# Optimization experiments

Hardware: AMD Instinct MI355X
Metric: run time of the kernel (lower is better)

## Reference

```python
import jax, jax.numpy as jnp
import numpy as np

CLUSTERS = 128
ITERATIONS = 10
TOPK = 32
NEG = -1e7


def setup_inputs() -> dict:
    key = jax.random.key(0)
    k1, k2, k3, k4 = jax.random.split(key, 4)
    N, L, H, E = 2, 2048, 8, 64
    BITS = 32
    return {
        "queries": jax.random.normal(k1, (N, L, H, E), dtype=jnp.float32),
        "keys": jax.random.normal(k2, (N, L, H, E), dtype=jnp.float32),
        "values": jax.random.normal(k3, (N, L, H, E), dtype=jnp.float32),
        "planes": jax.random.normal(k4, (BITS, E + 1), dtype=jnp.float32),
    }


def _cluster(bits, C, iterations):
    # bits: [N,H,L,B] in {0,1}. Lloyd k-means under Hamming distance.
    N, H, L, B = bits.shape
    init_idx = (np.arange(C) * L) // C
    cent = bits[:, :, init_idx, :]  # [N,H,C,B]
    for _ in range(iterations):
        # hamming(b,c) = b.(1-c) + (1-b).c
        d = (jnp.einsum('nhlb,nhcb->nhlc', bits, 1.0 - cent)
             + jnp.einsum('nhlb,nhcb->nhlc', 1.0 - bits, cent))
        assign = jnp.argmin(d, axis=-1)                      # [N,H,L]
        oh = jax.nn.one_hot(assign, C, dtype=jnp.float32)    # [N,H,L,C]
        cnt = oh.sum(axis=2)                                 # [N,H,C]
        sums = jnp.einsum('nhlc,nhlb->nhcb', oh, bits)
        new = (sums / jnp.maximum(cnt, 1.0)[..., None] >= 0.5).astype(jnp.float32)
        cent = jnp.where((cnt > 0.0)[..., None], new, cent)
    d = (jnp.einsum('nhlb,nhcb->nhlc', bits, 1.0 - cent)
         + jnp.einsum('nhlb,nhcb->nhlc', 1.0 - bits, cent))
    assign = jnp.argmin(d, axis=-1)
    oh = jax.nn.one_hot(assign, C, dtype=jnp.float32)
    cnt = oh.sum(axis=2)
    return assign, oh, cnt


def _forward(queries, keys, values, planes):
    # to [N,H,L,E]
    Q = jnp.transpose(queries, (0, 2, 1, 3))
    K = jnp.transpose(keys, (0, 2, 1, 3))
    V = jnp.transpose(values, (0, 2, 1, 3))
    N, H, L, E = Q.shape
    S = K.shape[2]
    temp = 1.0 / np.sqrt(E)

    # --- hash queries with random hyperplanes (bias column: hash_bias=True) ---
    x = jnp.concatenate([Q, jnp.ones(Q.shape[:-1] + (1,), Q.dtype)], axis=-1)
    bits = (jnp.einsum('nhle,be->nhlb', x, planes) > 0).astype(jnp.float32)

    # --- cluster queries (Lloyd on hamming distance over hash bits) ---
    assign, oh, cnt = _cluster(bits, CLUSTERS, ITERATIONS)

    # --- per-cluster centroid queries (mean over members) ---
    Qg = jnp.einsum('nhlc,nhle->nhce', oh, Q) / jnp.maximum(cnt, 1.0)[..., None]

    # --- top-k keys per cluster ---
    QKc = jnp.einsum('nhce,nhse->nhcs', Qg, K)   # [N,H,C,S]
    k = min(TOPK, S)
    _, tki = jax.lax.top_k(QKc, k)               # [N,H,C,k]

    # broadcast each cluster's top-k indices to its member queries
    idx_q = jnp.take_along_axis(
        tki, jnp.broadcast_to(assign[:, :, :, None], (N, H, L, k)), axis=2)  # [N,H,L,k]

    gather = jax.vmap(jax.vmap(lambda a, i: a[i]))
    K_sel = gather(K, idx_q)                     # [N,H,L,k,E]
    V_sel = gather(V, idx_q)                     # [N,H,L,k,E]

    qk = jnp.einsum('nhle,nhlke->nhlk', Q, K_sel)
    future = idx_q > jnp.arange(L)[None, None, :, None]   # causal: key pos > query pos
    qk = jnp.where(future, NEG, qk)
    A = jax.nn.softmax(temp * qk, axis=-1)
    A = A * (1.0 - future.astype(A.dtype))
    out = jnp.einsum('nhlk,nhlkd->nhld', A, V_sel)
    return jnp.transpose(out, (0, 2, 1, 3))      # [N,L,H,D]


def reference(queries, keys, values, planes):
    return _forward(queries, keys, values, planes)
```

## Files before the change

kernel.cpp:

```cpp
#include <hip/hip_runtime.h>
#include <math.h>

#define NB 2
#define HB 8
#define LB 2048
#define EB 64
#define BITSN 32
#define CLN 128
#define ITERS 10
#define TOPKN 32
#define NEGV -10000000.0f

typedef unsigned long long u64;
typedef unsigned int u32;

#define PART_NH16 (33 * 64)
#define PART_ITER16 (NB * HB * PART_NH16)
#define PART_TOTAL16 (ITERS * PART_ITER16)
#define BITS_BLOCKS 4096
#define ZBLOCKS ((PART_TOTAL16 + 255) / 256)

__global__ __launch_bounds__(256) void bits_zero_kernel(const float* __restrict__ q,
                                                        const float* __restrict__ planes,
                                                        u32* __restrict__ bits,
                                                        u32* __restrict__ zbuf) {
    int tid = threadIdx.x;
    int bid = blockIdx.x;
    if (bid >= BITS_BLOCKS) {
        int i = (bid - BITS_BLOCKS) * 256 + tid;
        if (i < PART_TOTAL16) zbuf[i] = 0u;
        return;
    }
    int wave = tid >> 6;
    int lane = tid & 63;
    int b = lane & 31;
    int which = lane >> 5;
    int qi = bid * 8 + wave * 2 + which;
    int l = qi & (LB - 1);
    int nh = qi / LB;
    int h = nh & (HB - 1);
    int n = nh / HB;
    const float* qrow = q + (((long long)n * LB + l) * HB + h) * EB;
    const float* prow = planes + b * (EB + 1);
    double acc = (double)prow[EB];
    #pragma unroll 8
    for (int e = 0; e < EB; ++e) acc += (double)qrow[e] * (double)prow[e];
    unsigned long long m = __ballot(acc > 0.0);
    if (b == 0) {
        bits[qi] = (u32)(which ? (m >> 32) : (m & 0xffffffffULL));
    }
}

__global__ __launch_bounds__(256) void kmeans_iter_kernel(const u32* __restrict__ bits,
                                                          const u32* __restrict__ part_prev,
                                                          u32* __restrict__ part_cur,
                                                          const u32* __restrict__ cent_prev_g,
                                                          u32* __restrict__ cent_cur_g,
                                                          int it) {
    __shared__ u32 cent[CLN];
    __shared__ int hist[33 * 128];
    int tid = threadIdx.x;
    int bid = blockIdx.x;
    int nh = bid >> 3;
    int tile = bid & 7;
    int lane = tid & 63;

    for (int i = tid; i < 33 * 128; i += 256) hist[i] = 0;
    if (tid < CLN) {
        u32 cv;
        if (it == 0) {
            cv = bits[nh * LB + tid * (LB / CLN)];
        } else {
            const u32* pp = part_prev + nh * PART_NH16;
            int sh = (tid & 1) * 16;
            int cnt = (int)((pp[32 * 64 + (tid >> 1)] >> sh) & 0xffffu);
            u32 nb = 0u;
            #pragma unroll
            for (int j = 0; j < BITSN; ++j) {
                int s = (int)((pp[j * 64 + (tid >> 1)] >> sh) & 0xffffu);
                if (2 * s >= cnt) nb |= (1u << j);
            }
            cv = (cnt > 0) ? nb : cent_prev_g[nh * CLN + tid];
        }
        cent[tid] = cv;
        if (tile == 0) cent_cur_g[nh * CLN + tid] = cv;
    }
    __syncthreads();

    int l = tile * 256 + tid;
    u32 bv = bits[nh * LB + l];

    u32 clo = cent[lane], chi = cent[lane + 64];
    u32 best = 0x7fffffffu;
    #pragma unroll 16
    for (int c = 0; c < 64; ++c) {
        u32 cc = (u32)__builtin_amdgcn_readlane((int)clo, c);
        u32 key = ((u32)__popc(bv ^ cc) << 7) | (u32)c;
        best = (key < best) ? key : best;
    }
    #pragma unroll 16
    for (int c = 0; c < 64; ++c) {
        u32 cc = (u32)__builtin_amdgcn_readlane((int)chi, c);
        u32 key = ((u32)__popc(bv ^ cc) << 7) | (u32)(64 + c);
        best = (key < best) ? key : best;
    }
    int bc = (int)(best & 127u);

    atomicAdd(&hist[32 * 128 + bc], 1);
    u32 bb = bv;
    while (bb) { int j = __ffs(bb) - 1; atomicAdd(&hist[j * 128 + bc], 1); bb &= bb - 1; }
    __syncthreads();

    u32* pc = part_cur + nh * PART_NH16;
    for (int i = tid; i < PART_NH16; i += 256) {
        int j = i >> 6, p = i & 63;
        u32 v = (u32)hist[j * 128 + 2 * p] | ((u32)hist[j * 128 + 2 * p + 1] << 16);
        if (v) atomicAdd(&pc[i], v);
    }
}

__global__ __launch_bounds__(1024) void list_final_kernel(const u32* __restrict__ bits,
                                                          const u32* __restrict__ part_prev,
                                                          const u32* __restrict__ cent_prev_g,
                                                          int* __restrict__ csort_g,
                                                          int* __restrict__ cnt_g,
                                                          int* __restrict__ ofs_g,
                                                          int* __restrict__ list_g) {
    __shared__ u32 cent[CLN];
    __shared__ int cnt[CLN];
    __shared__ int cntw[2][16][CLN];
    __shared__ int ofs[CLN];
    int nh = blockIdx.x;
    int tid = threadIdx.x;
    int w = tid >> 6, lane = tid & 63;

    if (tid < CLN) {
        const u32* pp = part_prev + nh * PART_NH16;
        int sh = (tid & 1) * 16;
        int cn = (int)((pp[32 * 64 + (tid >> 1)] >> sh) & 0xffffu);
        u32 nb = 0u;
        #pragma unroll
        for (int j = 0; j < BITSN; ++j) {
            int s = (int)((pp[j * 64 + (tid >> 1)] >> sh) & 0xffffu);
            if (2 * s >= cn) nb |= (1u << j);
        }
        cent[tid] = (cn > 0) ? nb : cent_prev_g[nh * CLN + tid];
        cnt[tid] = 0;
    }
    for (int i = tid; i < 2 * 16 * CLN; i += 1024) (&cntw[0][0][0])[i] = 0;
    __syncthreads();

    int l0 = tid, l1 = tid + 1024;
    u32 bv0 = bits[nh * LB + l0];
    u32 bv1 = bits[nh * LB + l1];
    u32 clo = cent[lane], chi = cent[lane + 64];
    u32 best0 = 0x7fffffffu, best1 = 0x7fffffffu;
    #pragma unroll 16
    for (int c = 0; c < 64; ++c) {
        u32 cc = (u32)__builtin_amdgcn_readlane((int)clo, c);
        u32 k0 = ((u32)__popc(bv0 ^ cc) << 7) | (u32)c;
        u32 k1 = ((u32)__popc(bv1 ^ cc) << 7) | (u32)c;
        best0 = (k0 < best0) ? k0 : best0;
        best1 = (k1 < best1) ? k1 : best1;
    }
    #pragma unroll 16
    for (int c = 0; c < 64; ++c) {
        u32 cc = (u32)__builtin_amdgcn_readlane((int)chi, c);
        u32 k0 = ((u32)__popc(bv0 ^ cc) << 7) | (u32)(64 + c);
        u32 k1 = ((u32)__popc(bv1 ^ cc) << 7) | (u32)(64 + c);
        best0 = (k0 < best0) ? k0 : best0;
        best1 = (k1 < best1) ? k1 : best1;
    }
    int bc0 = (int)(best0 & 127u);
    int bc1 = (int)(best1 & 127u);
    u64 ltmask = (lane == 0) ? 0ULL : (~0ULL >> (64 - lane));

    int rank0 = 0, rank1 = 0;
    for (int c = 0; c < CLN; ++c) {
        u64 m0 = __ballot(bc0 == c);
        u64 m1 = __ballot(bc1 == c);
        if ((m0 | m1) == 0ULL) continue;
        if (bc0 == c) rank0 = (int)__popcll(m0 & ltmask);
        if (bc1 == c) rank1 = (int)__popcll(m1 & ltmask);
        if (lane == 0) {
            int p0 = (int)__popcll(m0), p1 = (int)__popcll(m1);
            if (p0) cntw[0][w][c] = p0;
            if (p1) cntw[1][w][c] = p1;
            atomicAdd(&cnt[c], p0 + p1);
        }
    }
    __syncthreads();
    if (tid == 0) {
        int run = 0;
        for (int c = 0; c < CLN; ++c) { ofs[c] = run; run += cnt[c]; }
    }
    __syncthreads();
    if (tid < CLN) {
        int c = tid;
        int run = ofs[c];
        #pragma unroll
        for (int g = 0; g < 2; ++g)
            for (int ww = 0; ww < 16; ++ww) {
                int t = cntw[g][ww][c];
                cntw[g][ww][c] = run;
                run += t;
            }
        cnt_g[nh * CLN + c] = cnt[c];
        ofs_g[nh * CLN + c] = ofs[c];
    }
    __syncthreads();
    {
        int p0 = cntw[0][w][bc0] + rank0;
        int p1 = cntw[1][w][bc1] + rank1;
        list_g[nh * LB + p0] = l0;
        list_g[nh * LB + p1] = l1;
        csort_g[nh * LB + p0] = bc0;
        csort_g[nh * LB + p1] = bc1;
    }
}

__global__ __launch_bounds__(256) void qg_kernel(const float* __restrict__ q,
                                                 const int* __restrict__ cnt_g,
                                                 const int* __restrict__ ofs_g,
                                                 const int* __restrict__ list_g,
                                                 float* __restrict__ qgf) {
    __shared__ double ps[4][EB];
    int bid = blockIdx.x;
    int nh = bid >> 7;
    int h = nh & (HB - 1);
    int n = nh / HB;
    int tid = threadIdx.x;
    int w = tid >> 6, lane = tid & 63;
    int cn = cnt_g[bid];
    int o = ofs_g[bid];
    const int* lp = list_g + nh * LB + o;
    double acc = 0.0;
    for (int i = w; i < cn; i += 4) {
        int l = lp[i];
        acc += (double)q[(((long long)n * LB + l) * HB + h) * EB + lane];
    }
    ps[w][lane] = acc;
    __syncthreads();
    if (tid < EB) {
        double s = ((ps[0][tid] + ps[1][tid]) + ps[2][tid]) + ps[3][tid];
        double dcn = (double)(cn > 0 ? cn : 1);
        qgf[(long long)bid * EB + tid] = (float)(s / dcn);
    }
}

__global__ __launch_bounds__(256) void scores_kernel(const float* __restrict__ kk,
                                                     const float* __restrict__ qgf,
                                                     u32* __restrict__ keys) {
    __shared__ float qs[CLN * EB];
    int bid = blockIdx.x;
    int nh = bid >> 5;
    int tile = bid & 31;
    int h = nh & (HB - 1);
    int n = nh / HB;
    int tid = threadIdx.x;
    int w = tid >> 6;
    int lane = tid & 63;
    int l = tile * 64 + lane;
    int cbase = w * 32;

    {
        const float4* src = (const float4*)(qgf + (long long)nh * CLN * EB);
        float4* dst = (float4*)qs;
        #pragma unroll
        for (int i = 0; i < 8; ++i) dst[tid + 256 * i] = src[tid + 256 * i];
    }

    const float4* kr4 = (const float4*)(kk + (((long long)n * LB + l) * HB + h) * EB);
    float rr[EB];
    #pragma unroll
    for (int i = 0; i < 16; ++i) {
        float4 t4 = kr4[i];
        rr[4 * i] = t4.x; rr[4 * i + 1] = t4.y; rr[4 * i + 2] = t4.z; rr[4 * i + 3] = t4.w;
    }
    __syncthreads();

    for (int c = 0; c < 32; ++c) {
        const float4* qp = (const float4*)(qs + (cbase + c) * EB);
        float a0 = 0.f, a1 = 0.f, a2 = 0.f, a3 = 0.f;
        #pragma unroll
        for (int i = 0; i < 4; ++i) {
            float4 q0 = qp[i], q1 = qp[4 + i], q2 = qp[8 + i], q3 = qp[12 + i];
            int e0 = 4 * i, e1 = 16 + 4 * i, e2 = 32 + 4 * i, e3 = 48 + 4 * i;
            a0 = fmaf(q0.x, rr[e0], a0); a0 = fmaf(q0.y, rr[e0 + 1], a0);
            a0 = fmaf(q0.z, rr[e0 + 2], a0); a0 = fmaf(q0.w, rr[e0 + 3], a0);
            a1 = fmaf(q1.x, rr[e1], a1); a1 = fmaf(q1.y, rr[e1 + 1], a1);
            a1 = fmaf(q1.z, rr[e1 + 2], a1); a1 = fmaf(q1.w, rr[e1 + 3], a1);
            a2 = fmaf(q2.x, rr[e2], a2); a2 = fmaf(q2.y, rr[e2 + 1], a2);
            a2 = fmaf(q2.z, rr[e2 + 2], a2); a2 = fmaf(q2.w, rr[e2 + 3], a2);
            a3 = fmaf(q3.x, rr[e3], a3); a3 = fmaf(q3.y, rr[e3 + 1], a3);
            a3 = fmaf(q3.z, rr[e3 + 2], a3); a3 = fmaf(q3.w, rr[e3 + 3], a3);
        }
        float acc = (a0 + a1) + (a2 + a3);
        u32 u = __float_as_uint(acc);
        u = ((int)u < 0) ? ~u : (u | 0x80000000u);
        keys[((long long)(nh * CLN + cbase + c)) * LB + l] = u;
    }
}

__global__ __launch_bounds__(64) void topsel_kernel(const u32* __restrict__ keys,
                                                    int* __restrict__ tki_g) {
    int bid = blockIdx.x;
    int lane = threadIdx.x;
    const uint4* kp4 = (const uint4*)(keys + (long long)bid * LB);
    u64 k[32];
    #pragma unroll
    for (int t = 0; t < 8; ++t) {
        uint4 kv = kp4[lane + 64 * t];
        int l0 = (lane + 64 * t) * 4;
        k[4 * t]     = ((u64)kv.x << 32) | (u32)(2047 - l0);
        k[4 * t + 1] = ((u64)kv.y << 32) | (u32)(2047 - (l0 + 1));
        k[4 * t + 2] = ((u64)kv.z << 32) | (u32)(2047 - (l0 + 2));
        k[4 * t + 3] = ((u64)kv.w << 32) | (u32)(2047 - (l0 + 3));
    }
    u64 m0 = k[0], m1 = k[8], m2 = k[16], m3 = k[24];
    #pragma unroll
    for (int t = 1; t < 8; ++t) {
        if (k[t] > m0) m0 = k[t];
        if (k[8 + t] > m1) m1 = k[8 + t];
        if (k[16 + t] > m2) m2 = k[16 + t];
        if (k[24 + t] > m3) m3 = k[24 + t];
    }
    if (m1 > m0) m0 = m1;
    if (m3 > m2) m2 = m3;
    u64 cur = (m2 > m0) ? m2 : m0;

    for (int r = 0; r < TOPKN; ++r) {
        u64 wk = cur;
        #pragma unroll
        for (int off = 1; off < 64; off <<= 1) {
            u64 o = __shfl_xor(wk, off);
            if (o > wk) wk = o;
        }
        if (lane == 0) tki_g[bid * TOPKN + r] = 2047 - (int)(wk & 2047u);
        if (wk == cur) {
            u64 nm = 0ULL;
            #pragma unroll
            for (int t = 0; t < 32; ++t) {
                u64 kt = k[t];
                u64 cand = (kt < wk) ? kt : 0ULL;
                if (cand > nm) nm = cand;
            }
            cur = nm;
        }
    }
}

__device__ __forceinline__ void attn_one(const float* __restrict__ q,
                                         const float* __restrict__ kk,
                                         const float* __restrict__ vv,
                                         int n, int h, int l,
                                         const int* __restrict__ krow,
                                         int lane, float* __restrict__ out) {
    int j = lane & 31, p = lane >> 5;
    int kidx = krow[j];
    const float* vbase = vv + ((long long)n * LB * HB + h) * EB;
    float vreg[TOPKN];
    #pragma unroll
    for (int jj = 0; jj < TOPKN; ++jj) {
        int kj = __shfl(kidx, jj);
        vreg[jj] = vbase[(long long)kj * (HB * EB) + lane];
    }
    const float4* q4 = (const float4*)(q + (((long long)n * LB + l) * HB + h) * EB) + p * 8;
    const float4* k4 = (const float4*)(kk + (((long long)n * LB + kidx) * HB + h) * EB) + p * 8;
    float part = 0.f;
    #pragma unroll
    for (int i = 0; i < 8; ++i) {
        float4 a = q4[i], b = k4[i];
        part += a.x * b.x + a.y * b.y + a.z * b.z + a.w * b.w;
    }
    float qlo = __shfl(part, j);
    float qhi = __shfl(part, j + 32);
    float qk = qlo + qhi;
    bool future = kidx > l;
    float logit = 0.125f * (future ? NEGV : qk);
    float m = logit;
    #pragma unroll
    for (int off = 16; off; off >>= 1) m = fmaxf(m, __shfl_xor(m, off));
    float ex = expf(logit - m);
    float ssum = ex;
    #pragma unroll
    for (int off = 16; off; off >>= 1) ssum += __shfl_xor(ssum, off);
    float a = future ? 0.f : ex / ssum;
    float oacc = 0.f;
    #pragma unroll
    for (int jj = 0; jj < TOPKN; ++jj) {
        float aj = __shfl(a, jj);
        oacc = fmaf(aj, vreg[jj], oacc);
    }
    out[(((long long)n * LB + l) * HB + h) * EB + lane] = oacc;
}

__global__ __launch_bounds__(256) void attn_quad_kernel(const float* __restrict__ q,
                                                        const float* __restrict__ kk,
                                                        const float* __restrict__ vv,
                                                        const int* __restrict__ list_g,
                                                        const int* __restrict__ csort_g,
                                                        const int* __restrict__ tki_g,
                                                        float* __restrict__ out) {
    int tid = threadIdx.x;
    int wave = tid >> 6, lane = tid & 63;
    int idx = blockIdx.x * 4 + wave;
    int nh = idx >> 9;
    int qd = idx & 511;
    int pos = 4 * qd;
    int l0 = list_g[nh * LB + pos];
    int l1 = list_g[nh * LB + pos + 1];
    int l2 = list_g[nh * LB + pos + 2];
    int l3 = list_g[nh * LB + pos + 3];
    int c0 = csort_g[nh * LB + pos];
    int c1 = csort_g[nh * LB + pos + 1];
    int c2 = csort_g[nh * LB + pos + 2];
    int c3 = csort_g[nh * LB + pos + 3];
    int h = nh & (HB - 1);
    int n = nh / HB;

    if ((c0 != c1) | (c1 != c2) | (c2 != c3)) {
        attn_one(q, kk, vv, n, h, l0, tki_g + (nh * CLN + c0) * TOPKN, lane, out);
        attn_one(q, kk, vv, n, h, l1, tki_g + (nh * CLN + c1) * TOPKN, lane, out);
        attn_one(q, kk, vv, n, h, l2, tki_g + (nh * CLN + c2) * TOPKN, lane, out);
        attn_one(q, kk, vv, n, h, l3, tki_g + (nh * CLN + c3) * TOPKN, lane, out);
        return;
    }

    const int* krow = tki_g + (nh * CLN + c0) * TOPKN;
    int j = lane & 31, p = lane >> 5;
    int kidx = krow[j];
    const float* vbase = vv + ((long long)n * LB * HB + h) * EB;
    float vreg[TOPKN];
    #pragma unroll
    for (int jj = 0; jj < TOPKN; ++jj) {
        int kj = __shfl(kidx, jj);
        vreg[jj] = vbase[(long long)kj * (HB * EB) + lane];
    }

    const float4* q40 = (const float4*)(q + (((long long)n * LB + l0) * HB + h) * EB) + p * 8;
    const float4* q41 = (const float4*)(q + (((long long)n * LB + l1) * HB + h) * EB) + p * 8;
    const float4* q42 = (const float4*)(q + (((long long)n * LB + l2) * HB + h) * EB) + p * 8;
    const float4* q43 = (const float4*)(q + (((long long)n * LB + l3) * HB + h) * EB) + p * 8;
    const float4* k4  = (const float4*)(kk + (((long long)n * LB + kidx) * HB + h) * EB) + p * 8;
    float p0 = 0.f, p1 = 0.f, p2 = 0.f, p3 = 0.f;
    #pragma unroll
    for (int i = 0; i < 8; ++i) {
        float4 b = k4[i];
        float4 a0 = q40[i], a1 = q41[i], a2 = q42[i], a3 = q43[i];
        p0 += a0.x * b.x + a0.y * b.y + a0.z * b.z + a0.w * b.w;
        p1 += a1.x * b.x + a1.y * b.y + a1.z * b.z + a1.w * b.w;
        p2 += a2.x * b.x + a2.y * b.y + a2.z * b.z + a2.w * b.w;
        p3 += a3.x * b.x + a3.y * b.y + a3.z * b.z + a3.w * b.w;
    }
    float qk0 = __shfl(p0, j) + __shfl(p0, j + 32);
    float qk1 = __shfl(p1, j) + __shfl(p1, j + 32);
    float qk2 = __shfl(p2, j) + __shfl(p2, j + 32);
    float qk3 = __shfl(p3, j) + __shfl(p3, j + 32);

    bool f0 = kidx > l0, f1 = kidx > l1, f2 = kidx > l2, f3 = kidx > l3;
    float g0 = 0.125f * (f0 ? NEGV : qk0);
    float g1 = 0.125f * (f1 ? NEGV : qk1);
    float g2 = 0.125f * (f2 ? NEGV : qk2);
    float g3 = 0.125f * (f3 ? NEGV : qk3);
    float m0 = g0, m1 = g1, m2 = g2, m3 = g3;
    #pragma unroll
    for (int off = 16; off; off >>= 1) {
        m0 = fmaxf(m0, __shfl_xor(m0, off));
        m1 = fmaxf(m1, __shfl_xor(m1, off));
        m2 = fmaxf(m2, __shfl_xor(m2, off));
        m3 = fmaxf(m3, __shfl_xor(m3, off));
    }
    float e0 = expf(g0 - m0), e1 = expf(g1 - m1);
    float e2 = expf(g2 - m2), e3 = expf(g3 - m3);
    float s0 = e0, s1 = e1, s2 = e2, s3 = e3;
    #pragma unroll
    for (int off = 16; off; off >>= 1) {
        s0 += __shfl_xor(s0, off);
        s1 += __shfl_xor(s1, off);
        s2 += __shfl_xor(s2, off);
        s3 += __shfl_xor(s3, off);
    }
    float a0 = f0 ? 0.f : e0 / s0;
    float a1 = f1 ? 0.f : e1 / s1;
    float a2 = f2 ? 0.f : e2 / s2;
    float a3 = f3 ? 0.f : e3 / s3;

    float o0 = 0.f, o1 = 0.f, o2 = 0.f, o3 = 0.f;
    #pragma unroll
    for (int jj = 0; jj < TOPKN; ++jj) {
        float v = vreg[jj];
        o0 = fmaf(__shfl(a0, jj), v, o0);
        o1 = fmaf(__shfl(a1, jj), v, o1);
        o2 = fmaf(__shfl(a2, jj), v, o2);
        o3 = fmaf(__shfl(a3, jj), v, o3);
    }
    out[(((long long)n * LB + l0) * HB + h) * EB + lane] = o0;
    out[(((long long)n * LB + l1) * HB + h) * EB + lane] = o1;
    out[(((long long)n * LB + l2) * HB + h) * EB + lane] = o2;
    out[(((long long)n * LB + l3) * HB + h) * EB + lane] = o3;
}

extern "C" void kernel_launch(void* const* d_in, const int* in_sizes, int n_in,
                              void* d_out, int out_size, void* d_ws, size_t ws_size,
                              hipStream_t stream) {
    const float* q = (const float*)d_in[0];
    const float* k = (const float*)d_in[1];
    const float* v = (const float*)d_in[2];
    const float* planes = (const float*)d_in[3];
    float* out = (float*)d_out;

    const int NQ = NB * HB * LB;
    char* ws = (char*)d_ws;
    u32* bits     = (u32*)(ws);
    int* csort_g  = (int*)(ws + 0x20000);
    int* cnt_g    = (int*)(ws + 0x40000);
    int* ofs_g    = (int*)(ws + 0x42000);
    int* list_g   = (int*)(ws + 0x44000);
    float* qgf    = (float*)(ws + 0x64000);
    int* tki_g    = (int*)(ws + 0xE4000);
    u32* keys     = (u32*)(ws + 0x124000);
    u32* part_all = (u32*)(ws + 0x124000);
    u32* cents0   = (u32*)(ws + 0x124000 + 0x180000);
    u32* cents1   = (u32*)(ws + 0x124000 + 0x182000);

    bits_zero_kernel<<<BITS_BLOCKS + ZBLOCKS, 256, 0, stream>>>(q, planes, bits, part_all);

    for (int it = 0; it < ITERS; ++it) {
        const u32* pp = part_all + (it == 0 ? 0 : (it - 1)) * PART_ITER16;
        u32* pc       = part_all + it * PART_ITER16;
        const u32* cprev = (it & 1) ? cents0 : cents1;
        u32* ccur        = (it & 1) ? cents1 : cents0;
        kmeans_iter_kernel<<<NB * HB * 8, 256, 0, stream>>>(bits, pp, pc, cprev, ccur, it);
    }
    list_final_kernel<<<NB * HB, 1024, 0, stream>>>(
        bits, part_all + 9 * PART_ITER16, cents1, csort_g, cnt_g, ofs_g, list_g);
    qg_kernel<<<NB * HB * CLN, 256, 0, stream>>>(q, cnt_g, ofs_g, list_g, qgf);
    scores_kernel<<<NB * HB * 32, 256, 0, stream>>>(k, qgf, keys);
    topsel_kernel<<<NB * HB * CLN, 64, 0, stream>>>(keys, tki_g);
    attn_quad_kernel<<<NQ / 16, 256, 0, stream>>>(q, k, v, list_g, csort_g, tki_g, out);
}
```

Measured before the change: 250.1 us.

## Fuse cluster scoring with top-k selection in LDS; pair same-cluster queries

Merges the centroid-key scoring kernel and the top-k selection kernel into one kernel. Each block now handles 8 clusters for one head, keeps the 8x2048 score keys in shared memory and runs top-k on them there, so the global keys buffer and one launch go away. In exchange each block reloads all 2048 keys for every group of 8 clusters, which means 16 times more K reads per head and fewer blocks (256). Separately, mixed-cluster quads in attention now process same-cluster pairs together so the V gather and the key-row loads are shared between the two queries.

```diff
diff --git a/kernel.cpp b/kernel.cpp
--- a/kernel.cpp
+++ b/kernel.cpp
@@ -248,104 +248,101 @@
     }
 }
 
-__global__ __launch_bounds__(256) void scores_kernel(const float* __restrict__ kk,
-                                                     const float* __restrict__ qgf,
-                                                     u32* __restrict__ keys) {
-    __shared__ float qs[CLN * EB];
+__global__ __launch_bounds__(256) void scores_topsel_kernel(const float* __restrict__ kk,
+                                                            const float* __restrict__ qgf,
+                                                            int* __restrict__ tki_g) {
+    __shared__ float qs[8 * EB];
+    __shared__ u32 skey[8][LB];
     int bid = blockIdx.x;
-    int nh = bid >> 5;
-    int tile = bid & 31;
+    int nh = bid >> 4;
+    int g = bid & 15;
+    int cbase = g * 8;
     int h = nh & (HB - 1);
     int n = nh / HB;
     int tid = threadIdx.x;
-    int w = tid >> 6;
-    int lane = tid & 63;
-    int l = tile * 64 + lane;
-    int cbase = w * 32;
-
-    {
-        const float4* src = (const float4*)(qgf + (long long)nh * CLN * EB);
-        float4* dst = (float4*)qs;
+    int w = tid >> 6, lane = tid & 63;
+
+    if (tid < 128)
+        ((float4*)qs)[tid] = ((const float4*)(qgf + (long long)(nh * CLN + cbase) * EB))[tid];
+    __syncthreads();
+
+    for (int step = 0; step < 8; ++step) {
+        int l = step * 256 + tid;
+        const float4* kr4 = (const float4*)(kk + (((long long)n * LB + l) * HB + h) * EB);
+        float rr[EB];
         #pragma unroll
-        for (int i = 0; i < 8; ++i) dst[tid + 256 * i] = src[tid + 256 * i];
-    }
-
-    const float4* kr4 = (const float4*)(kk + (((long long)n * LB + l) * HB + h) * EB);
-    float rr[EB];
-    #pragma unroll
-    for (int i = 0; i < 16; ++i) {
-        float4 t4 = kr4[i];
-        rr[4 * i] = t4.x; rr[4 * i + 1] = t4.y; rr[4 * i + 2] = t4.z; rr[4 * i + 3] = t4.w;
-    }
-    __syncthreads();
-
-    for (int c = 0; c < 32; ++c) {
-        const float4* qp = (const float4*)(qs + (cbase + c) * EB);
-        float a0 = 0.f, a1 = 0.f, a2 = 0.f, a3 = 0.f;
+        for (int i = 0; i < 16; ++i) {
+            float4 t4 = kr4[i];
+            rr[4 * i] = t4.x; rr[4 * i + 1] = t4.y; rr[4 * i + 2] = t4.z; rr[4 * i + 3] = t4.w;
+        }
         #pragma unroll
-        for (int i = 0; i < 4; ++i) {
-            float4 q0 = qp[i], q1 = qp[4 + i], q2 = qp[8 + i], q3 = qp[12 + i];
-            int e0 = 4 * i, e1 = 16 + 4 * i, e2 = 32 + 4 * i, e3 = 48 + 4 * i;
-            a0 = fmaf(q0.x, rr[e0], a0); a0 = fmaf(q0.y, rr[e0 + 1], a0);
-            a0 = fmaf(q0.z, rr[e0 + 2], a0); a0 = fmaf(q0.w, rr[e0 + 3], a0);
-            a1 = fmaf(q1.x, rr[e1], a1); a1 = fmaf(q1.y, rr[e1 + 1], a1);
-            a1 = fmaf(q1.z, rr[e1 + 2], a1); a1 = fmaf(q1.w, rr[e1 + 3], a1);
-            a2 = fmaf(q2.x, rr[e2], a2); a2 = fmaf(q2.y, rr[e2 + 1], a2);
-            a2 = fmaf(q2.z, rr[e2 + 2], a2); a2 = fmaf(q2.w, rr[e2 + 3], a2);
-            a3 = fmaf(q3.x, rr[e3], a3); a3 = fmaf(q3.y, rr[e3 + 1], a3);
-            a3 = fmaf(q3.z, rr[e3 + 2], a3); a3 = fmaf(q3.w, rr[e3 + 3], a3);
-        }
-        float acc = (a0 + a1) + (a2 + a3);
-        u32 u = __float_as_uint(acc);
-        u = ((int)u < 0) ? ~u : (u | 0x80000000u);
-        keys[((long long)(nh * CLN + cbase + c)) * LB + l] = u;
-    }
-}
-
-__global__ __launch_bounds__(64) void topsel_kernel(const u32* __restrict__ keys,
-                                                    int* __restrict__ tki_g) {
-    int bid = blockIdx.x;
-    int lane = threadIdx.x;
-    const uint4* kp4 = (const uint4*)(keys + (long long)bid * LB);
-    u64 k[32];
-    #pragma unroll
-    for (int t = 0; t < 8; ++t) {
-        uint4 kv = kp4[lane + 64 * t];
-        int l0 = (lane + 64 * t) * 4;
-        k[4 * t]     = ((u64)kv.x << 32) | (u32)(2047 - l0);
-        k[4 * t + 1] = ((u64)kv.y << 32) | (u32)(2047 - (l0 + 1));
-        k[4 * t + 2] = ((u64)kv.z << 32) | (u32)(2047 - (l0 + 2));
-        k[4 * t + 3] = ((u64)kv.w << 32) | (u32)(2047 - (l0 + 3));
-    }
-    u64 m0 = k[0], m1 = k[8], m2 = k[16], m3 = k[24];
-    #pragma unroll
-    for (int t = 1; t < 8; ++t) {
-        if (k[t] > m0) m0 = k[t];
-        if (k[8 + t] > m1) m1 = k[8 + t];
-        if (k[16 + t] > m2) m2 = k[16 + t];
-        if (k[24 + t] > m3) m3 = k[24 + t];
-    }
-    if (m1 > m0) m0 = m1;
-    if (m3 > m2) m2 = m3;
-    u64 cur = (m2 > m0) ? m2 : m0;
-
-    for (int r = 0; r < TOPKN; ++r) {
-        u64 wk = cur;
+        for (int c = 0; c < 8; ++c) {
+            const float4* qp = (const float4*)(qs + c * EB);
+            float a0 = 0.f, a1 = 0.f, a2 = 0.f, a3 = 0.f;
+            #pragma unroll
+            for (int i = 0; i < 4; ++i) {
+                float4 q0 = qp[i], q1 = qp[4 + i], q2 = qp[8 + i], q3 = qp[12 + i];
+                int e0 = 4 * i, e1 = 16 + 4 * i, e2 = 32 + 4 * i, e3 = 48 + 4 * i;
+                a0 = fmaf(q0.x, rr[e0], a0); a0 = fmaf(q0.y, rr[e0 + 1], a0);
+                a0 = fmaf(q0.z, rr[e0 + 2], a0); a0 = fmaf(q0.w, rr[e0 + 3], a0);
+                a1 = fmaf(q1.x, rr[e1], a1); a1 = fmaf(q1.y, rr[e1 + 1], a1);
+                a1 = fmaf(q1.z, rr[e1 + 2], a1); a1 = fmaf(q1.w, rr[e1 + 3], a1);
+                a2 = fmaf(q2.x, rr[e2], a2); a2 = fmaf(q2.y, rr[e2 + 1], a2);
+                a2 = fmaf(q2.z, rr[e2 + 2], a2); a2 = fmaf(q2.w, rr[e2 + 3], a2);
+                a3 = fmaf(q3.x, rr[e3], a3); a3 = fmaf(q3.y, rr[e3 + 1], a3);
+                a3 = fmaf(q3.z, rr[e3 + 2], a3); a3 = fmaf(q3.w, rr[e3 + 3], a3);
+            }
+            float acc = (a0 + a1) + (a2 + a3);
+            u32 u = __float_as_uint(acc);
+            u = ((int)u < 0) ? ~u : (u | 0x80000000u);
+            skey[c][l] = u;
+        }
+    }
+    __syncthreads();
+
+    for (int rep = 0; rep < 2; ++rep) {
+        int c = w + rep * 4;
+        const uint4* kp4 = (const uint4*)&skey[c][0];
+        u64 k[32];
         #pragma unroll
-        for (int off = 1; off < 64; off <<= 1) {
-            u64 o = __shfl_xor(wk, off);
-            if (o > wk) wk = o;
-        }
-        if (lane == 0) tki_g[bid * TOPKN + r] = 2047 - (int)(wk & 2047u);
-        if (wk == cur) {
-            u64 nm = 0ULL;
+        for (int t = 0; t < 8; ++t) {
+            uint4 kv = kp4[lane + 64 * t];
+            int l0 = (lane + 64 * t) * 4;
+            k[4 * t]     = ((u64)kv.x << 32) | (u32)(2047 - l0);
+            k[4 * t + 1] = ((u64)kv.y << 32) | (u32)(2047 - (l0 + 1));
+            k[4 * t + 2] = ((u64)kv.z << 32) | (u32)(2047 - (l0 + 2));
+            k[4 * t + 3] = ((u64)kv.w << 32) | (u32)(2047 - (l0 + 3));
+        }
+        u64 m0 = k[0], m1 = k[8], m2 = k[16], m3 = k[24];
+        #pragma unroll
+        for (int t = 1; t < 8; ++t) {
+            if (k[t] > m0) m0 = k[t];
+            if (k[8 + t] > m1) m1 = k[8 + t];
+            if (k[16 + t] > m2) m2 = k[16 + t];
+            if (k[24 + t] > m3) m3 = k[24 + t];
+        }
+        if (m1 > m0) m0 = m1;
+        if (m3 > m2) m2 = m3;
+        u64 cur = (m2 > m0) ? m2 : m0;
+        for (int r = 0; r < TOPKN; ++r) {
+            u64 wk = cur;
             #pragma unroll
-            for (int t = 0; t < 32; ++t) {
-                u64 kt = k[t];
-                u64 cand = (kt < wk) ? kt : 0ULL;
-                if (cand > nm) nm = cand;
+            for (int off = 1; off < 64; off <<= 1) {
+                u64 o = __shfl_xor(wk, off);
+                if (o > wk) wk = o;
             }
-            cur = nm;
+            if (lane == 0)
+                tki_g[(nh * CLN + cbase + c) * TOPKN + r] = 2047 - (int)(wk & 2047u);
+            if (wk == cur) {
+                u64 nm = 0ULL;
+                #pragma unroll
+                for (int t = 0; t < 32; ++t) {
+                    u64 kt = k[t];
+                    u64 cand = (kt < wk) ? kt : 0ULL;
+                    if (cand > nm) nm = cand;
+                }
+                cur = nm;
+            }
         }
     }
 }
@@ -393,6 +390,64 @@
         oacc = fmaf(aj, vreg[jj], oacc);
     }
     out[(((long long)n * LB + l) * HB + h) * EB + lane] = oacc;
+}
+
+__device__ __forceinline__ void attn_pair_body(const float* __restrict__ q,
+                                               const float* __restrict__ kk,
+                                               const float* __restrict__ vv,
+                                               int n, int h, int l0, int l1,
+                                               const int* __restrict__ krow,
+                                               int lane, float* __restrict__ out) {
+    int j = lane & 31, p = lane >> 5;
+    int kidx = krow[j];
+    const float* vbase = vv + ((long long)n * LB * HB + h) * EB;
+    float vreg[TOPKN];
+    #pragma unroll
+    for (int jj = 0; jj < TOPKN; ++jj) {
+        int kj = __shfl(kidx, jj);
+        vreg[jj] = vbase[(long long)kj * (HB * EB) + lane];
+    }
+    const float4* q40 = (const float4*)(q + (((long long)n * LB + l0) * HB + h) * EB) + p * 8;
+    const float4* q41 = (const float4*)(q + (((long long)n * LB + l1) * HB + h) * EB) + p * 8;
+    const float4* k4  = (const float4*)(kk + (((long long)n * LB + kidx) * HB + h) * EB) + p * 8;
+    float part0 = 0.f, part1 = 0.f;
+    #pragma unroll
+    for (int i = 0; i < 8; ++i) {
+        float4 b = k4[i];
+        float4 a0 = q40[i], a1 = q41[i];
+        part0 += a0.x * b.x + a0.y * b.y + a0.z * b.z + a0.w * b.w;
+        part1 += a1.x * b.x + a1.y * b.y + a1.z * b.z + a1.w * b.w;
+    }
+    float qk0 = __shfl(part0, j) + __shfl(part0, j + 32);
+    float qk1 = __shfl(part1, j) + __shfl(part1, j + 32);
+    bool fut0 = kidx > l0, fut1 = kidx > l1;
+    float lg0 = 0.125f * (fut0 ? NEGV : qk0);
+    float lg1 = 0.125f * (fut1 ? NEGV : qk1);
+    float m0 = lg0, m1 = lg1;
+    #pragma unroll
+    for (int off = 16; off; off >>= 1) {
+        m0 = fmaxf(m0, __shfl_xor(m0, off));
+        m1 = fmaxf(m1, __shfl_xor(m1, off));
+    }
+    float e0 = expf(lg0 - m0), e1 = expf(lg1 - m1);
+    float s0 = e0, s1 = e1;
+    #pragma unroll
+    for (int off = 16; off; off >>= 1) {
+        s0 += __shfl_xor(s0, off);
+        s1 += __shfl_xor(s1, off);
+    }
+    float a0 = fut0 ? 0.f : e0 / s0;
+    float a1 = fut1 ? 0.f : e1 / s1;
+    float o0 = 0.f, o1 = 0.f;
+    #pragma unroll
+    for (int jj = 0; jj < TOPKN; ++jj) {
+        float aj0 = __shfl(a0, jj);
+        float aj1 = __shfl(a1, jj);
+        o0 = fmaf(aj0, vreg[jj], o0);
+        o1 = fmaf(aj1, vreg[jj], o1);
+    }
+    out[(((long long)n * LB + l0) * HB + h) * EB + lane] = o0;
+    out[(((long long)n * LB + l1) * HB + h) * EB + lane] = o1;
 }
 
 __global__ __launch_bounds__(256) void attn_quad_kernel(const float* __restrict__ q,
@@ -420,10 +475,18 @@
     int n = nh / HB;
 
     if ((c0 != c1) | (c1 != c2) | (c2 != c3)) {
-        attn_one(q, kk, vv, n, h, l0, tki_g + (nh * CLN + c0) * TOPKN, lane, out);
-        attn_one(q, kk, vv, n, h, l1, tki_g + (nh * CLN + c1) * TOPKN, lane, out);
-        attn_one(q, kk, vv, n, h, l2, tki_g + (nh * CLN + c2) * TOPKN, lane, out);
-        attn_one(q, kk, vv, n, h, l3, tki_g + (nh * CLN + c3) * TOPKN, lane, out);
+        if (c0 == c1) {
+            attn_pair_body(q, kk, vv, n, h, l0, l1, tki_g + (nh * CLN + c0) * TOPKN, lane, out);
+        } else {
+            attn_one(q, kk, vv, n, h, l0, tki_g + (nh * CLN + c0) * TOPKN, lane, out);
+            attn_one(q, kk, vv, n, h, l1, tki_g + (nh * CLN + c1) * TOPKN, lane, out);
+        }
+        if (c2 == c3) {
+            attn_pair_body(q, kk, vv, n, h, l2, l3, tki_g + (nh * CLN + c2) * TOPKN, lane, out);
+        } else {
+            attn_one(q, kk, vv, n, h, l2, tki_g + (nh * CLN + c2) * TOPKN, lane, out);
+            attn_one(q, kk, vv, n, h, l3, tki_g + (nh * CLN + c3) * TOPKN, lane, out);
+        }
         return;
     }
 
@@ -519,7 +582,6 @@
     int* list_g   = (int*)(ws + 0x44000);
     float* qgf    = (float*)(ws + 0x64000);
     int* tki_g    = (int*)(ws + 0xE4000);
-    u32* keys     = (u32*)(ws + 0x124000);
     u32* part_all = (u32*)(ws + 0x124000);
     u32* cents0   = (u32*)(ws + 0x124000 + 0x180000);
     u32* cents1   = (u32*)(ws + 0x124000 + 0x182000);
@@ -536,7 +598,6 @@
     list_final_kernel<<<NB * HB, 1024, 0, stream>>>(
         bits, part_all + 9 * PART_ITER16, cents1, csort_g, cnt_g, ofs_g, list_g);
     qg_kernel<<<NB * HB * CLN, 256, 0, stream>>>(q, cnt_g, ofs_g, list_g, qgf);
-    scores_kernel<<<NB * HB * 32, 256, 0, stream>>>(k, qgf, keys);
-    topsel_kernel<<<NB * HB * CLN, 64, 0, stream>>>(keys, tki_g);
+    scores_topsel_kernel<<<NB * HB * 16, 256, 0, stream>>>(k, qgf, tki_g);
     attn_quad_kernel<<<NQ / 16, 256, 0, stream>>>(q, k, v, list_g, csort_g, tki_g, out);
 }
```

New measurement: 276.3 us. 10.5% more time.
